# Kernel tuning notes

Measured on AMD Instinct MI355X. Metric: run time of the kernel, lower is better.

The kernel has to match this reference:

```python
import jax, jax.numpy as jnp
import numpy as np
import math

D_MODEL = 1024
NUM_HEADS = 16
B, L = 2, 2048
# scale_level=0, patch_time_span=1 -> effective_stride=1
PERIODS = (1.0, 30.0)
WEIGHTS = (0.8, 0.4)
SIGMAS = (0.5, 2.0)


def setup_inputs() -> dict:
    key = jax.random.key(0)
    ks = jax.random.split(key, 10)
    s = 1.0 / math.sqrt(D_MODEL)
    inp = {
        "x": jax.random.normal(ks[0], (B, L, D_MODEL), dtype=jnp.float32),
        "Wq": jax.random.normal(ks[1], (D_MODEL, D_MODEL), dtype=jnp.float32) * s,
        "bq": jax.random.normal(ks[2], (D_MODEL,), dtype=jnp.float32) * 0.01,
        "Wk": jax.random.normal(ks[3], (D_MODEL, D_MODEL), dtype=jnp.float32) * s,
        "bk": jax.random.normal(ks[4], (D_MODEL,), dtype=jnp.float32) * 0.01,
        "Wv": jax.random.normal(ks[5], (D_MODEL, D_MODEL), dtype=jnp.float32) * s,
        "bv": jax.random.normal(ks[6], (D_MODEL,), dtype=jnp.float32) * 0.01,
        "Wo": jax.random.normal(ks[7], (D_MODEL, D_MODEL), dtype=jnp.float32) * s,
        "bo": jax.random.normal(ks[8], (D_MODEL,), dtype=jnp.float32) * 0.01,
        "prior_lambda": jnp.asarray(2.0, dtype=jnp.float32),
    }
    return inp


def _gaussian_mask(length):
    idx = jnp.arange(length, dtype=jnp.float32)
    delta = jnp.abs(idx[:, None] - idx[None, :])  # [L, L]
    mask = jnp.zeros_like(delta)
    for p, w, sigma in zip(PERIODS, WEIGHTS, SIGMAS):
        if p < 0.2:
            continue
        mask = mask + w * jnp.exp(-((delta - p) ** 2) / (2.0 * sigma ** 2))
    return mask


def reference(x, Wq, bq, Wk, bk, Wv, bv, Wo, bo, prior_lambda):
    Bx, Lx, D = x.shape
    H = NUM_HEADS
    hd = D // H

    def split_heads(t):  # [B, L, D] -> [B, H, L, hd]
        return t.reshape(Bx, Lx, H, hd).transpose(0, 2, 1, 3)

    Q = split_heads(x @ Wq.T + bq)
    K = split_heads(x @ Wk.T + bk)
    V = split_heads(x @ Wv.T + bv)

    scores = jnp.einsum("bhqd,bhkd->bhqk", Q, K) / math.sqrt(hd)
    scores = scores + prior_lambda * _gaussian_mask(Lx)[None, None, :, :]
    attn = jax.nn.softmax(scores, axis=-1)
    out = jnp.einsum("bhqk,bhkd->bhqd", attn, V)
    out = out.transpose(0, 2, 1, 3).reshape(Bx, Lx, D)
    return out @ Wo.T + bo
```

## Files before the change

### kernel.cpp

```cpp
#include <hip/hip_runtime.h>

#define D_MODEL 1024
#define SEQ_L   2048
#define NHEADS  16
#define HDIM    64
#define NROWS   4096

#define QSCALE 0.18033688011112042f
#define LOG2E  1.4426950408889634f

#if __has_builtin(__builtin_amdgcn_exp2f)
#define EXP2F(x) __builtin_amdgcn_exp2f(x)
#else
#define EXP2F(x) __expf((x) * 0.6931471805599453f)
#endif

typedef __attribute__((ext_vector_type(8))) short short8;
typedef __attribute__((ext_vector_type(4))) short short4v;
typedef __attribute__((ext_vector_type(4))) float floatx4;
typedef __attribute__((ext_vector_type(4))) unsigned short ushort4v;
typedef unsigned short ushort;

static __device__ __forceinline__ ushort f2bf(float f) {
    unsigned int u = __float_as_uint(f);
    u += 0x7FFFu + ((u >> 16) & 1u);
    return (ushort)(u >> 16);
}

static __device__ __forceinline__ floatx4 mfma16(short8 a, short8 b, floatx4 c) {
    return __builtin_amdgcn_mfma_f32_16x16x32_bf16(a, b, c, 0, 0, 0);
}

static __device__ __forceinline__ void store8bf(ushort* dst, float4 a, float4 b) {
    uint4 pk;
    pk.x = (unsigned)f2bf(a.x) | ((unsigned)f2bf(a.y) << 16);
    pk.y = (unsigned)f2bf(a.z) | ((unsigned)f2bf(a.w) << 16);
    pk.z = (unsigned)f2bf(b.x) | ((unsigned)f2bf(b.y) << 16);
    pk.w = (unsigned)f2bf(b.z) | ((unsigned)f2bf(b.w) << 16);
    *(uint4*)dst = pk;
}

static __device__ __forceinline__ void gll16(const ushort* g, ushort* l) {
    __builtin_amdgcn_global_load_lds(
        (const __attribute__((address_space(1))) unsigned int*)(const unsigned int*)g,
        (__attribute__((address_space(3))) unsigned int*)(unsigned int*)l,
        16, 0, 0);
}

__global__ __launch_bounds__(256) void convert_bf16(
    const float* __restrict__ x,
    const float* __restrict__ wq, const float* __restrict__ wk,
    const float* __restrict__ wv, const float* __restrict__ wo,
    ushort* __restrict__ xb, ushort* __restrict__ wb3, ushort* __restrict__ wob)
{
    const int seg = blockIdx.y;
    const float* src;
    ushort* dst;
    int n;
    if      (seg == 0) { src = x;  dst = xb;                n = 4194304; }
    else if (seg == 1) { src = wq; dst = wb3;               n = 1048576; }
    else if (seg == 2) { src = wk; dst = wb3 + 1048576;     n = 1048576; }
    else if (seg == 3) { src = wv; dst = wb3 + 2097152;     n = 1048576; }
    else               { src = wo; dst = wob;               n = 1048576; }
    const int i = (blockIdx.x * 256 + threadIdx.x) * 8;
    if (i >= n) return;
    float4 a = *(const float4*)(src + i);
    float4 b = *(const float4*)(src + i + 4);
    store8bf(dst + i, a, b);
}

__global__ __launch_bounds__(256, 4) void gemm_qkv(
    const ushort* __restrict__ A, const ushort* __restrict__ B,
    const float* __restrict__ bq, const float* __restrict__ bk,
    const float* __restrict__ bv,
    ushort* __restrict__ Qo, ushort* __restrict__ Ko, ushort* __restrict__ Vo)
{
    __shared__ ushort As[64 * 64];
    __shared__ ushort Bs[128 * 64];

    const int tid  = threadIdx.x;
    const int w    = tid >> 6;
    const int lane = tid & 63;
    const int l15  = lane & 15;
    const int quad = lane >> 4;

    const int bm = blockIdx.y * 64;
    const int bn = blockIdx.x * 128;
    const int z  = blockIdx.x >> 3;

    const int ciA0 = tid,        ciA1 = tid + 256;
    const int rA0 = ciA0 >> 3,   rA1 = ciA1 >> 3;
    const int sA0i = ciA0 & 7,   sA1i = ciA1 & 7;
    const ushort* aP0 = A + (size_t)(bm + rA0) * 1024 + (sA0i ^ (rA0 & 7)) * 8;
    const ushort* aP1 = A + (size_t)(bm + rA1) * 1024 + (sA1i ^ (rA1 & 7)) * 8;
    ushort* lA0 = &As[rA0 * 64 + sA0i * 8];
    ushort* lA1 = &As[rA1 * 64 + sA1i * 8];

    const ushort* bP[4];
    ushort* lB[4];
#pragma unroll
    for (int p = 0; p < 4; p++) {
        const int ci = tid + p * 256;
        const int r = ci >> 3, s = ci & 7;
        bP[p] = B + (size_t)(bn + r) * 1024 + (s ^ (r & 7)) * 8;
        lB[p] = &Bs[r * 64 + s * 8];
    }

    const int x7 = l15 & 7;

    floatx4 acc[4][2];
#pragma unroll
    for (int i = 0; i < 4; i++)
#pragma unroll
        for (int j = 0; j < 2; j++) acc[i][j] = (floatx4){0.f, 0.f, 0.f, 0.f};

    for (int k0 = 0; k0 < 1024; k0 += 64) {
        __syncthreads();
        gll16(aP0 + k0, lA0);
        gll16(aP1 + k0, lA1);
#pragma unroll
        for (int p = 0; p < 4; p++) gll16(bP[p] + k0, lB[p]);
        __syncthreads();

#pragma unroll
        for (int kk = 0; kk < 2; kk++) {
            const int slot = ((kk * 4 + quad) ^ x7) * 8;
            short8 af[4], bf[2];
#pragma unroll
            for (int mi = 0; mi < 4; mi++)
                af[mi] = *(const short8*)&As[(mi * 16 + l15) * 64 + slot];
#pragma unroll
            for (int ni = 0; ni < 2; ni++)
                bf[ni] = *(const short8*)&Bs[(w * 32 + ni * 16 + l15) * 64 + slot];
            if (z == 2) {
#pragma unroll
                for (int mi = 0; mi < 4; mi++)
#pragma unroll
                    for (int ni = 0; ni < 2; ni++)
                        acc[mi][ni] = mfma16(af[mi], bf[ni], acc[mi][ni]);
            } else {
#pragma unroll
                for (int mi = 0; mi < 4; mi++)
#pragma unroll
                    for (int ni = 0; ni < 2; ni++)
                        acc[mi][ni] = mfma16(bf[ni], af[mi], acc[mi][ni]);
            }
        }
    }

    __syncthreads();
    ushort* St = Bs;
    const int cwbase = bn & 1023;
    const int bb = bm >> 11;

    if (z == 2) {
#pragma unroll
        for (int ni = 0; ni < 2; ni++) {
            const int hdp = w * 32 + ni * 16 + l15;
            const float bvl = bv[cwbase + hdp];
            const int xr = (hdp & 7) << 1;
#pragma unroll
            for (int mi = 0; mi < 4; mi++) {
                ushort4v pk;
#pragma unroll
                for (int r = 0; r < 4; r++) pk[r] = f2bf(acc[mi][ni][r] + bvl);
                const int gs = (mi * 4 + quad) ^ xr;
                *(ushort4v*)&St[hdp * 64 + gs * 4] = pk;
            }
        }
        __syncthreads();
        const int li0 = bm & 2047;
        const int c = lane & 7;
#pragma unroll
        for (int t = 0; t < 4; t++) {
            const int hdp = w * 32 + t * 8 + (lane >> 3);
            const int h  = (cwbase >> 6) + (hdp >> 6);
            const int hd = hdp & 63;
            const int gs = (2 * c) ^ ((hdp & 7) << 1);
            uint4 vdat = *(const uint4*)&St[hdp * 64 + gs * 4];
            *(uint4*)(Vo + ((size_t)(bb * NHEADS + h) * HDIM + hd) * SEQ_L + li0 + c * 8) = vdat;
        }
    } else {
        const float* bias = z ? bk : bq;
        const float scale = z ? 1.0f : QSCALE;
        ushort* outp = z ? Ko : Qo;
#pragma unroll
        for (int ni = 0; ni < 2; ni++) {
            const int colw = cwbase + w * 32 + ni * 16 + quad * 4;
            const float4 bb4 = *(const float4*)&bias[colw];
#pragma unroll
            for (int mi = 0; mi < 4; mi++) {
                const int row = mi * 16 + l15;
                ushort4v pk;
                pk[0] = f2bf((acc[mi][ni][0] + bb4.x) * scale);
                pk[1] = f2bf((acc[mi][ni][1] + bb4.y) * scale);
                pk[2] = f2bf((acc[mi][ni][2] + bb4.z) * scale);
                pk[3] = f2bf((acc[mi][ni][3] + bb4.w) * scale);
                const int gs = (w * 8 + ni * 4 + quad) ^ ((row & 7) << 2);
                *(ushort4v*)&St[row * 128 + gs * 4] = pk;
            }
        }
        __syncthreads();
        const int c = l15;
        const int h0 = cwbase >> 6;
        const int h  = h0 + (c >> 3);
        const int hd0 = (c & 7) * 8;
#pragma unroll
        for (int t = 0; t < 4; t++) {
            const int row = w * 16 + t * 4 + quad;
            const int li = (bm + row) & 2047;
            const int gs = (2 * c) ^ ((row & 7) << 2);
            uint4 vdat = *(const uint4*)&St[row * 128 + gs * 4];
            *(uint4*)(outp + ((size_t)(bb * NHEADS + h) * SEQ_L + li) * HDIM + hd0) = vdat;
        }
    }
}

__global__ __launch_bounds__(512, 4) void attn(
    const ushort* __restrict__ Q,
    const ushort* __restrict__ K,
    const ushort* __restrict__ Vt,
    const float* __restrict__ lam,
    ushort* __restrict__ Aout)
{
    __shared__ float mtab[128];
    __shared__ ushort Ks[3][64 * 64];
    __shared__ ushort Vts[3][64 * 64];
    __shared__ float olred[512];

    const int tid  = threadIdx.x;
    const int wave = tid >> 6;
    const int ws   = wave & 3;
    const int ks   = wave >> 2;
    const int lane = tid & 63;
    const int l15  = lane & 15;
    const int quad = lane >> 4;

    const int bid = blockIdx.x;
    const int swz = (bid & 7) * 64 + (bid >> 3);
    const int qb = swz & 15;
    const int h  = (swz >> 4) & 15;
    const int bz = swz >> 8;
    const int bh = bz * NHEADS + h;
    const int q0 = qb * 128;

    const float lambda = *lam;
    if (tid < 128) {
        float d  = (float)tid;
        float e1 = (d - 1.f) * (d - 1.f);
        float e2 = (d - 30.f) * (d - 30.f);
        mtab[tid] = LOG2E * lambda *
                    (0.8f * __expf(-2.0f * e1) + 0.4f * __expf(-0.125f * e2));
    }

    const ushort* qp =
        Q + ((size_t)bh * SEQ_L + q0 + ws * 16 + l15) * HDIM + quad * 8;
    short8 qf[2][2];
    qf[0][0] = *(const short8*)qp;
    qf[0][1] = *(const short8*)(qp + 32);
    qf[1][0] = *(const short8*)(qp + 64 * HDIM);
    qf[1][1] = *(const short8*)(qp + 64 * HDIM + 32);

    const ushort* kbase = K  + ((size_t)bh * SEQ_L) * HDIM;
    const ushort* vbase = Vt + ((size_t)bh * HDIM) * SEQ_L;

    const int cid = tid;
    const int rowc = cid >> 3;
    const int clc  = (cid & 7) ^ (rowc & 7);
    const ushort* kg = kbase + (size_t)rowc * HDIM + clc * 8;
    const ushort* vg = vbase + (size_t)rowc * SEQ_L + clc * 8;

    floatx4 o[2][4];
#pragma unroll
    for (int g = 0; g < 2; g++)
#pragma unroll
        for (int i = 0; i < 4; i++) o[g][i] = (floatx4){0.f, 0.f, 0.f, 0.f};
    floatx4 ol[2];
    ol[0] = (floatx4){0.f, 0.f, 0.f, 0.f};
    ol[1] = (floatx4){0.f, 0.f, 0.f, 0.f};

    uint4 onesw;
    onesw.x = 0x3F803F80u; onesw.y = 0x3F803F80u;
    onesw.z = 0x3F803F80u; onesw.w = 0x3F803F80u;
    const short8 ones8 = __builtin_bit_cast(short8, onesw);

    __syncthreads();

    gll16(kg, &Ks[0][cid * 8]);
    gll16(vg, &Vts[0][cid * 8]);
    gll16(kg + (size_t)64 * HDIM, &Ks[1][cid * 8]);
    gll16(vg + 64, &Vts[1][cid * 8]);

    const int xo  = l15 & 7;
    const int nt0 = ks * 2;

    for (int t = 0; t < 32; t++) {
        int cur = t % 3;
        if (t < 31) asm volatile("s_waitcnt vmcnt(2)" ::: "memory");
        else        asm volatile("s_waitcnt vmcnt(0)" ::: "memory");
        __builtin_amdgcn_sched_barrier(0);
        __builtin_amdgcn_s_barrier();
        if (t + 2 < 32) {
            int nb = cur + 2; if (nb >= 3) nb -= 3;
            const int koff = (t + 2) * 64;
            gll16(kg + (size_t)koff * HDIM, &Ks[nb][cid * 8]);
            gll16(vg + koff, &Vts[nb][cid * 8]);
        }

        floatx4 s[2][2];
#pragma unroll
        for (int g = 0; g < 2; g++)
#pragma unroll
            for (int j = 0; j < 2; j++) s[g][j] = (floatx4){0.f, 0.f, 0.f, 0.f};
        __builtin_amdgcn_s_setprio(1);
#pragma unroll
        for (int kk = 0; kk < 2; kk++) {
            const int slot = (kk * 4 + quad) ^ xo;
#pragma unroll
            for (int j = 0; j < 2; j++) {
                const int nt = nt0 + j;
                short8 kf = *(const short8*)&Ks[cur][(nt * 16 + l15) * 64 + slot * 8];
                s[0][j] = mfma16(kf, qf[0][kk], s[0][j]);
                s[1][j] = mfma16(kf, qf[1][kk], s[1][j]);
            }
        }
        __builtin_amdgcn_s_setprio(0);

#pragma unroll
        for (int g = 0; g < 2; g++) {
            const int tg = t - (qb * 2 + g);
            if (tg >= -1 && tg <= 1) {
                const int qg = q0 + g * 64 + ws * 16 + l15;
#pragma unroll
                for (int j = 0; j < 2; j++) {
                    const int kgi = t * 64 + (nt0 + j) * 16 + quad * 4;
#pragma unroll
                    for (int r = 0; r < 4; r++) {
                        int dq = qg - (kgi + r);
                        int ad = dq < 0 ? -dq : dq;
                        s[g][j][r] += mtab[ad];
                    }
                }
            }
        }

        short8 pb8[2];
#pragma unroll
        for (int g = 0; g < 2; g++) {
            unsigned ur[8];
#pragma unroll
            for (int r = 0; r < 4; r++)
                ur[r] = __float_as_uint(EXP2F(s[g][0][r])) + 0x8000u;
#pragma unroll
            for (int r = 0; r < 4; r++)
                ur[4 + r] = __float_as_uint(EXP2F(s[g][1][r])) + 0x8000u;
            uint4 pk;
            pk.x = __builtin_amdgcn_perm(ur[1], ur[0], 0x07060302u);
            pk.y = __builtin_amdgcn_perm(ur[3], ur[2], 0x07060302u);
            pk.z = __builtin_amdgcn_perm(ur[5], ur[4], 0x07060302u);
            pk.w = __builtin_amdgcn_perm(ur[7], ur[6], 0x07060302u);
            pb8[g] = __builtin_bit_cast(short8, pk);
        }

        const int glo = ((ks << 2) + (quad >> 1)) ^ xo;
        const int ghi = glo ^ 2;
        __builtin_amdgcn_s_setprio(1);
#pragma unroll
        for (int nt = 0; nt < 4; nt++) {
            const int rb = (nt * 16 + l15) * 64 + (quad & 1) * 4;
            short4v vlo = *(const short4v*)&Vts[cur][rb + glo * 8];
            short4v vhi = *(const short4v*)&Vts[cur][rb + ghi * 8];
            short8 vf8 = __builtin_shufflevector(vlo, vhi, 0, 1, 2, 3, 4, 5, 6, 7);
            o[0][nt] = mfma16(vf8, pb8[0], o[0][nt]);
            o[1][nt] = mfma16(vf8, pb8[1], o[1][nt]);
        }
        ol[0] = mfma16(ones8, pb8[0], ol[0]);
        ol[1] = mfma16(ones8, pb8[1], ol[1]);
        __builtin_amdgcn_s_setprio(0);
    }

    __syncthreads();
    float* redb = (ws < 2) ? (float*)&Ks[0][0] : (float*)&Vts[0][0];
    const int wsl = ws & 1;
    if (ks == 1) {
#pragma unroll
        for (int g = 0; g < 2; g++) {
#pragma unroll
            for (int nt = 0; nt < 4; nt++)
                *(floatx4*)&redb[wsl * 2048 + ((g * 4 + nt) * 64 + lane) * 4] = o[g][nt];
            olred[((ws * 2 + g) * 64) + lane] = ol[g][0];
        }
    }
    __syncthreads();
    if (ks == 0) {
#pragma unroll
        for (int g = 0; g < 2; g++) {
            const float l = ol[g][0] + olred[((ws * 2 + g) * 64) + lane];
            const float linv = 1.0f / l;
            const int qg = q0 + g * 64 + ws * 16 + l15;
            ushort* obase = Aout + ((size_t)bz * SEQ_L + qg) * D_MODEL + h * HDIM;
#pragma unroll
            for (int nt = 0; nt < 4; nt++) {
                floatx4 op = *(const floatx4*)&redb[wsl * 2048 + ((g * 4 + nt) * 64 + lane) * 4];
                ushort4v pk;
#pragma unroll
                for (int r = 0; r < 4; r++) pk[r] = f2bf((o[g][nt][r] + op[r]) * linv);
                *(ushort4v*)(obase + nt * 16 + quad * 4) = pk;
            }
        }
    }
}

__global__ __launch_bounds__(256, 4) void gemm_out(
    const ushort* __restrict__ A, const ushort* __restrict__ B,
    const float* __restrict__ bo, float* __restrict__ out)
{
    __shared__ ushort As[64 * 64];
    __shared__ ushort Bs[64 * 64];

    const int tid  = threadIdx.x;
    const int w    = tid >> 6;
    const int lane = tid & 63;
    const int l15  = lane & 15;
    const int quad = lane >> 4;

    const int bm = blockIdx.y * 64;
    const int bn = blockIdx.x * 64;

    const int ci0 = tid, ci1 = tid + 256;
    const int r0 = ci0 >> 3, r1 = ci1 >> 3;
    const int s0 = ci0 & 7,  s1 = ci1 & 7;
    const ushort* aP0 = A + (size_t)(bm + r0) * 1024 + (s0 ^ (r0 & 7)) * 8;
    const ushort* aP1 = A + (size_t)(bm + r1) * 1024 + (s1 ^ (r1 & 7)) * 8;
    const ushort* bP0 = B + (size_t)(bn + r0) * 1024 + (s0 ^ (r0 & 7)) * 8;
    const ushort* bP1 = B + (size_t)(bn + r1) * 1024 + (s1 ^ (r1 & 7)) * 8;
    ushort* lA0 = &As[r0 * 64 + s0 * 8];
    ushort* lA1 = &As[r1 * 64 + s1 * 8];
    ushort* lB0 = &Bs[r0 * 64 + s0 * 8];
    ushort* lB1 = &Bs[r1 * 64 + s1 * 8];

    const int x7 = l15 & 7;

    floatx4 acc[4];
#pragma unroll
    for (int i = 0; i < 4; i++) acc[i] = (floatx4){0.f, 0.f, 0.f, 0.f};

    for (int k0 = 0; k0 < 1024; k0 += 64) {
        __syncthreads();
        gll16(aP0 + k0, lA0);
        gll16(aP1 + k0, lA1);
        gll16(bP0 + k0, lB0);
        gll16(bP1 + k0, lB1);
        __syncthreads();

#pragma unroll
        for (int kk = 0; kk < 2; kk++) {
            const int slot = ((kk * 4 + quad) ^ x7) * 8;
            short8 bf = *(const short8*)&Bs[(w * 16 + l15) * 64 + slot];
#pragma unroll
            for (int mi = 0; mi < 4; mi++) {
                short8 af = *(const short8*)&As[(mi * 16 + l15) * 64 + slot];
                acc[mi] = mfma16(bf, af, acc[mi]);
            }
        }
    }

    const int col0 = bn + w * 16 + quad * 4;
    const float4 bb4 = *(const float4*)&bo[col0];
#pragma unroll
    for (int mi = 0; mi < 4; mi++) {
        const int row = bm + mi * 16 + l15;
        float4 st;
        st.x = acc[mi][0] + bb4.x;
        st.y = acc[mi][1] + bb4.y;
        st.z = acc[mi][2] + bb4.z;
        st.w = acc[mi][3] + bb4.w;
        *(float4*)(out + (size_t)row * 1024 + col0) = st;
    }
}

extern "C" void kernel_launch(void* const* d_in, const int* in_sizes, int n_in,
                              void* d_out, int out_size, void* d_ws, size_t ws_size,
                              hipStream_t stream)
{
    const float* x   = (const float*)d_in[0];
    const float* Wq  = (const float*)d_in[1];
    const float* bq  = (const float*)d_in[2];
    const float* Wk  = (const float*)d_in[3];
    const float* bk  = (const float*)d_in[4];
    const float* Wv  = (const float*)d_in[5];
    const float* bv  = (const float*)d_in[6];
    const float* Wo  = (const float*)d_in[7];
    const float* bo  = (const float*)d_in[8];
    const float* lam = (const float*)d_in[9];
    float* out = (float*)d_out;

    const size_t NELEM = (size_t)NROWS * D_MODEL;
    ushort* Qw  = (ushort*)d_ws;
    ushort* Kw  = Qw + NELEM;
    ushort* Vw  = Kw + NELEM;
    ushort* XA  = Vw + NELEM;
    ushort* Wb3 = XA + NELEM;
    ushort* Wob = Wb3 + 3 * 1024 * 1024;

    dim3 gc(2048, 5);
    convert_bf16<<<gc, 256, 0, stream>>>(x, Wq, Wk, Wv, Wo, XA, Wb3, Wob);

    dim3 g1(3072 / 128, NROWS / 64);
    gemm_qkv<<<g1, 256, 0, stream>>>(XA, Wb3, bq, bk, bv, Qw, Kw, Vw);

    attn<<<512, 512, 0, stream>>>(Qw, Kw, Vw, lam, XA);

    dim3 g3(1024 / 64, NROWS / 64);
    gemm_out<<<g3, 256, 0, stream>>>(XA, Wob, bo, out);
}
```

Measured before the change: 190.0 us.

## Use 128-key double-buffered tiles in attention with per-half key split

Replaces the triple-buffered 64-key K/V pipeline with a double-buffered 128-key tile per iteration, halving loop trips and barriers. Each key-half wave group now handles a full 64-key subtile rather than interleaved 16-key slices, and the V tile uses a 16-way XOR swizzle for a 128-wide row. This cuts barrier and loop overhead per key and gives more MFMA work between syncs. In exchange there is less prefetch depth, since only one tile is in flight, and it relies on a plain __syncthreads without explicit vmcnt waits for the async loads.

```diff
diff --git a/kernel.cpp b/kernel.cpp
--- a/kernel.cpp
+++ b/kernel.cpp
@@ -224,14 +224,14 @@
     ushort* __restrict__ Aout)
 {
     __shared__ float mtab[128];
-    __shared__ ushort Ks[3][64 * 64];
-    __shared__ ushort Vts[3][64 * 64];
+    __shared__ ushort Ks[2][128 * 64];
+    __shared__ ushort Vts[2][64 * 128];
     __shared__ float olred[512];
 
     const int tid  = threadIdx.x;
     const int wave = tid >> 6;
     const int ws   = wave & 3;
-    const int ks   = wave >> 2;
+    const int kh   = wave >> 2;
     const int lane = tid & 63;
     const int l15  = lane & 15;
     const int quad = lane >> 4;
@@ -264,11 +264,19 @@
     const ushort* kbase = K  + ((size_t)bh * SEQ_L) * HDIM;
     const ushort* vbase = Vt + ((size_t)bh * HDIM) * SEQ_L;
 
-    const int cid = tid;
-    const int rowc = cid >> 3;
-    const int clc  = (cid & 7) ^ (rowc & 7);
-    const ushort* kg = kbase + (size_t)rowc * HDIM + clc * 8;
-    const ushort* vg = vbase + (size_t)rowc * SEQ_L + clc * 8;
+    const int kr0 = tid >> 3,          kr1 = (tid + 512) >> 3;
+    const int ksl0 = tid & 7,          ksl1 = tid & 7;
+    const ushort* kg0 = kbase + (size_t)kr0 * HDIM + (ksl0 ^ (kr0 & 7)) * 8;
+    const ushort* kg1 = kbase + (size_t)kr1 * HDIM + (ksl1 ^ (kr1 & 7)) * 8;
+    const int kl0 = kr0 * 64 + ksl0 * 8;
+    const int kl1 = kr1 * 64 + ksl1 * 8;
+
+    const int vr0 = tid >> 4,          vr1 = (tid + 512) >> 4;
+    const int vsl0 = tid & 15,         vsl1 = tid & 15;
+    const ushort* vg0 = vbase + (size_t)vr0 * SEQ_L + (vsl0 ^ (vr0 & 15)) * 8;
+    const ushort* vg1 = vbase + (size_t)vr1 * SEQ_L + (vsl1 ^ (vr1 & 15)) * 8;
+    const int vl0 = vr0 * 128 + vsl0 * 8;
+    const int vl1 = vr1 * 128 + vsl1 * 8;
 
     floatx4 o[2][4];
 #pragma unroll
@@ -284,40 +292,37 @@
     onesw.z = 0x3F803F80u; onesw.w = 0x3F803F80u;
     const short8 ones8 = __builtin_bit_cast(short8, onesw);
 
-    __syncthreads();
-
-    gll16(kg, &Ks[0][cid * 8]);
-    gll16(vg, &Vts[0][cid * 8]);
-    gll16(kg + (size_t)64 * HDIM, &Ks[1][cid * 8]);
-    gll16(vg + 64, &Vts[1][cid * 8]);
+    gll16(kg0, &Ks[0][kl0]);
+    gll16(kg1, &Ks[0][kl1]);
+    gll16(vg0, &Vts[0][vl0]);
+    gll16(vg1, &Vts[0][vl1]);
 
     const int xo  = l15 & 7;
-    const int nt0 = ks * 2;
-
-    for (int t = 0; t < 32; t++) {
-        int cur = t % 3;
-        if (t < 31) asm volatile("s_waitcnt vmcnt(2)" ::: "memory");
-        else        asm volatile("s_waitcnt vmcnt(0)" ::: "memory");
-        __builtin_amdgcn_sched_barrier(0);
-        __builtin_amdgcn_s_barrier();
-        if (t + 2 < 32) {
-            int nb = cur + 2; if (nb >= 3) nb -= 3;
-            const int koff = (t + 2) * 64;
-            gll16(kg + (size_t)koff * HDIM, &Ks[nb][cid * 8]);
-            gll16(vg + koff, &Vts[nb][cid * 8]);
-        }
-
-        floatx4 s[2][2];
+    const int nt0 = kh * 4;
+
+    for (int t = 0; t < 16; t++) {
+        const int cur = t & 1;
+        __syncthreads();
+        if (t + 1 < 16) {
+            const int nb = cur ^ 1;
+            const size_t ko = (size_t)(t + 1) * 128;
+            gll16(kg0 + ko * HDIM, &Ks[nb][kl0]);
+            gll16(kg1 + ko * HDIM, &Ks[nb][kl1]);
+            gll16(vg0 + ko, &Vts[nb][vl0]);
+            gll16(vg1 + ko, &Vts[nb][vl1]);
+        }
+
+        floatx4 s[2][4];
 #pragma unroll
         for (int g = 0; g < 2; g++)
 #pragma unroll
-            for (int j = 0; j < 2; j++) s[g][j] = (floatx4){0.f, 0.f, 0.f, 0.f};
+            for (int j = 0; j < 4; j++) s[g][j] = (floatx4){0.f, 0.f, 0.f, 0.f};
         __builtin_amdgcn_s_setprio(1);
 #pragma unroll
         for (int kk = 0; kk < 2; kk++) {
             const int slot = (kk * 4 + quad) ^ xo;
 #pragma unroll
-            for (int j = 0; j < 2; j++) {
+            for (int j = 0; j < 4; j++) {
                 const int nt = nt0 + j;
                 short8 kf = *(const short8*)&Ks[cur][(nt * 16 + l15) * 64 + slot * 8];
                 s[0][j] = mfma16(kf, qf[0][kk], s[0][j]);
@@ -326,14 +331,15 @@
         }
         __builtin_amdgcn_s_setprio(0);
 
+        const int t64 = 2 * t + kh;
 #pragma unroll
         for (int g = 0; g < 2; g++) {
-            const int tg = t - (qb * 2 + g);
+            const int tg = t64 - (qb * 2 + g);
             if (tg >= -1 && tg <= 1) {
                 const int qg = q0 + g * 64 + ws * 16 + l15;
 #pragma unroll
-                for (int j = 0; j < 2; j++) {
-                    const int kgi = t * 64 + (nt0 + j) * 16 + quad * 4;
+                for (int j = 0; j < 4; j++) {
+                    const int kgi = t64 * 64 + j * 16 + quad * 4;
 #pragma unroll
                     for (int r = 0; r < 4; r++) {
                         int dq = qg - (kgi + r);
@@ -344,45 +350,52 @@
             }
         }
 
-        short8 pb8[2];
+        short8 pb8[2][2];
 #pragma unroll
         for (int g = 0; g < 2; g++) {
-            unsigned ur[8];
-#pragma unroll
-            for (int r = 0; r < 4; r++)
-                ur[r] = __float_as_uint(EXP2F(s[g][0][r])) + 0x8000u;
-#pragma unroll
-            for (int r = 0; r < 4; r++)
-                ur[4 + r] = __float_as_uint(EXP2F(s[g][1][r])) + 0x8000u;
-            uint4 pk;
-            pk.x = __builtin_amdgcn_perm(ur[1], ur[0], 0x07060302u);
-            pk.y = __builtin_amdgcn_perm(ur[3], ur[2], 0x07060302u);
-            pk.z = __builtin_amdgcn_perm(ur[5], ur[4], 0x07060302u);
-            pk.w = __builtin_amdgcn_perm(ur[7], ur[6], 0x07060302u);
-            pb8[g] = __builtin_bit_cast(short8, pk);
-        }
-
-        const int glo = ((ks << 2) + (quad >> 1)) ^ xo;
-        const int ghi = glo ^ 2;
+#pragma unroll
+            for (int c = 0; c < 2; c++) {
+                unsigned ur[8];
+#pragma unroll
+                for (int r = 0; r < 4; r++)
+                    ur[r] = __float_as_uint(EXP2F(s[g][2 * c][r])) + 0x8000u;
+#pragma unroll
+                for (int r = 0; r < 4; r++)
+                    ur[4 + r] = __float_as_uint(EXP2F(s[g][2 * c + 1][r])) + 0x8000u;
+                uint4 pk;
+                pk.x = __builtin_amdgcn_perm(ur[1], ur[0], 0x07060302u);
+                pk.y = __builtin_amdgcn_perm(ur[3], ur[2], 0x07060302u);
+                pk.z = __builtin_amdgcn_perm(ur[5], ur[4], 0x07060302u);
+                pk.w = __builtin_amdgcn_perm(ur[7], ur[6], 0x07060302u);
+                pb8[g][c] = __builtin_bit_cast(short8, pk);
+            }
+        }
+
         __builtin_amdgcn_s_setprio(1);
 #pragma unroll
-        for (int nt = 0; nt < 4; nt++) {
-            const int rb = (nt * 16 + l15) * 64 + (quad & 1) * 4;
-            short4v vlo = *(const short4v*)&Vts[cur][rb + glo * 8];
-            short4v vhi = *(const short4v*)&Vts[cur][rb + ghi * 8];
-            short8 vf8 = __builtin_shufflevector(vlo, vhi, 0, 1, 2, 3, 4, 5, 6, 7);
-            o[0][nt] = mfma16(vf8, pb8[0], o[0][nt]);
-            o[1][nt] = mfma16(vf8, pb8[1], o[1][nt]);
-        }
-        ol[0] = mfma16(ones8, pb8[0], ol[0]);
-        ol[1] = mfma16(ones8, pb8[1], ol[1]);
+        for (int c = 0; c < 2; c++) {
+            const int cc = kh * 2 + c;
+            const int glo = (cc * 4 + (quad >> 1)) ^ l15;
+            const int ghi = glo ^ 2;
+#pragma unroll
+            for (int nt = 0; nt < 4; nt++) {
+                const int rb = (nt * 16 + l15) * 128 + (quad & 1) * 4;
+                short4v vlo = *(const short4v*)&Vts[cur][rb + glo * 8];
+                short4v vhi = *(const short4v*)&Vts[cur][rb + ghi * 8];
+                short8 vf8 = __builtin_shufflevector(vlo, vhi, 0, 1, 2, 3, 4, 5, 6, 7);
+                o[0][nt] = mfma16(vf8, pb8[0][c], o[0][nt]);
+                o[1][nt] = mfma16(vf8, pb8[1][c], o[1][nt]);
+            }
+            ol[0] = mfma16(ones8, pb8[0][c], ol[0]);
+            ol[1] = mfma16(ones8, pb8[1][c], ol[1]);
+        }
         __builtin_amdgcn_s_setprio(0);
     }
 
     __syncthreads();
     float* redb = (ws < 2) ? (float*)&Ks[0][0] : (float*)&Vts[0][0];
     const int wsl = ws & 1;
-    if (ks == 1) {
+    if (kh == 1) {
 #pragma unroll
         for (int g = 0; g < 2; g++) {
 #pragma unroll
@@ -392,7 +405,7 @@
         }
     }
     __syncthreads();
-    if (ks == 0) {
+    if (kh == 0) {
 #pragma unroll
         for (int g = 0; g < 2; g++) {
             const float l = ol[g][0] + olred[((ws * 2 + g) * 64) + lane];
```

New measurement: 188.5 us (median of 2 runs). About the same (-0.8%).
